# Kernel tuning notes

Hardware: AMD Instinct MI355X
Metric: run time of the kernel (lower is better)

The kernel has to match this reference:

```python
import jax, jax.numpy as jnp
import numpy as np
import math

B, L, DX, DH, DFF, N, M = 16, 1024, 2, 512, 2048, 3, 8
DK = DH // M  # 64
EPS = 1e-5


def batchnorm_pos(z):
    # fresh nn.BatchNorm1d(L, affine=False) in train mode on [B, L, DH]:
    # per-position (dim 1) mean/var over (batch, feature) axes, biased variance
    mu = jnp.mean(z, axis=(0, 2), keepdims=True)
    var = jnp.mean(jnp.square(z - mu), axis=(0, 2), keepdims=True)
    return (z - mu) / jnp.sqrt(var + EPS)


def setup_inputs() -> dict:
    key = jax.random.key(0)
    ks = jax.random.split(key, 13)
    s = lambda k, shape, scale: jax.random.normal(k, shape, dtype=jnp.float32) * scale
    return {
        "x": s(ks[0], (B, L, DX), 1.0),
        "Wh": s(ks[1], (DH, DX), 1.0 / math.sqrt(DX)),
        "bh": s(ks[2], (DH,), 0.02),
        "Wq": s(ks[3], (N, M, DK, DH), 1.0 / math.sqrt(DH)),
        "Wk": s(ks[4], (N, M, DK, DH), 1.0 / math.sqrt(DH)),
        "Wv": s(ks[5], (N, M, DK, DH), 1.0 / math.sqrt(DH)),
        "Wo": s(ks[6], (N, M, DH, DK), 1.0 / math.sqrt(DK)),
        "w_bn": s(ks[7], (N, DH), 1.0),
        "b_bn": s(ks[8], (N, DH), 1.0),
        "Wff0": s(ks[9], (N, DFF, DH), 1.0 / math.sqrt(DH)),
        "bff0": s(ks[10], (N, DFF), 0.02),
        "Wff1": s(ks[11], (N, DH, DFF), 1.0 / math.sqrt(DFF)),
        "bff1": s(ks[12], (N, DH), 0.02),
    }


def reference(x, Wh, bh, Wq, Wk, Wv, Wo, w_bn, b_bn, Wff0, bff0, Wff1, bff1):
    n_layers = Wq.shape[0]
    dk = Wq.shape[2]
    scale = 1.0 / math.sqrt(dk)
    h = jnp.einsum("bld,ed->ble", x, Wh) + bh  # [B, L, DH]
    for n in range(n_layers):
        # batched multi-head attention (replaces per-head python loop)
        q = jnp.einsum("bld,mkd->bmlk", h, Wq[n])  # [B, M, L, DK]
        k = jnp.einsum("bld,mkd->bmlk", h, Wk[n])
        v = jnp.einsum("bld,mvd->bmlv", h, Wv[n])
        scores = jnp.einsum("bmlk,bmjk->bmlj", q, k) * scale  # [B, M, L, L]
        attn = jax.nn.softmax(scores, axis=-1)
        t = jnp.einsum("bmlj,bmjv->bmlv", attn, v)
        h_mha = jnp.einsum("bmlv,mdv->bld", t, Wo[n])  # sum over heads
        h_bn = w_bn[n] * batchnorm_pos(h + h_mha) + b_bn[n]
        ff = jnp.einsum("blf,df->bld", jax.nn.relu(jnp.einsum("bld,fd->blf", h_bn, Wff0[n]) + bff0[n]), Wff1[n]) + bff1[n]
        h = w_bn[n] * batchnorm_pos(h_bn + ff) + b_bn[n]
    return h
```

## Files before the change

### kernel.cpp

```cpp
#include <hip/hip_runtime.h>
#include <hip/hip_bf16.h>
#include <math.h>

#define B_   16
#define L_   1024
#define BL_  16384
#define DH_  512
#define DFF_ 2048
#define NL_  3
#define M_   8
#define DK_  64

typedef __attribute__((ext_vector_type(8))) short bf16x8;
typedef __attribute__((ext_vector_type(4))) float f32x4;
typedef __attribute__((ext_vector_type(4))) unsigned short us4;
typedef __attribute__((ext_vector_type(8))) unsigned short us8;

__device__ __forceinline__ unsigned short f2b(float x) {
    __hip_bfloat16 h = __float2bfloat16(x);
    return *(unsigned short*)&h;
}
__device__ __forceinline__ float b2f(unsigned short u) {
    unsigned int v = ((unsigned int)u) << 16;
    return __builtin_bit_cast(float, v);
}

#define GLDS(g, l) __builtin_amdgcn_global_load_lds( \
        (const __attribute__((address_space(1))) unsigned int*)(const void*)(g), \
        (__attribute__((address_space(3))) unsigned int*)(void*)(l), 16, 0, 0)

#define QKV_T 2359296
#define WO_T  786432
#define FF_T  3145728
__global__ __launch_bounds__(256) void wprep_kernel(
    const float* __restrict__ Wq, const float* __restrict__ Wk,
    const float* __restrict__ Wv, const float* __restrict__ Wo,
    const float* __restrict__ Wff0, const float* __restrict__ Wff1,
    unsigned short* __restrict__ wqkvb3, unsigned short* __restrict__ wob3,
    unsigned short* __restrict__ wff0b3, unsigned short* __restrict__ wff1b3)
{
    int i4 = (blockIdx.x * 256 + threadIdx.x) * 4;
    const float* src;
    unsigned short* dst;
    if (i4 < QKV_T) {
        int n = i4 / 786432, r = i4 % 786432;
        if (r < 262144)      src = Wq + (size_t)n * 262144 + r;
        else if (r < 524288) src = Wk + (size_t)n * 262144 + r - 262144;
        else                 src = Wv + (size_t)n * 262144 + r - 524288;
        dst = wqkvb3 + i4;
    } else if (i4 < QKV_T + WO_T) {
        int i = i4 - QKV_T;
        int n = i / 262144, r = i % 262144;
        int d = r >> 9, mv = r & 511, mm = mv >> 6, vv = mv & 63;
        src = Wo + (size_t)n * 262144 + ((size_t)mm * 512 + d) * 64 + vv;
        dst = wob3 + i;
    } else if (i4 < QKV_T + WO_T + FF_T) {
        int i = i4 - QKV_T - WO_T;
        src = Wff0 + i;
        dst = wff0b3 + i;
    } else {
        int i = i4 - QKV_T - WO_T - FF_T;
        src = Wff1 + i;
        dst = wff1b3 + i;
    }
    float4 v = *(const float4*)src;
    us4 o;
    o.x = f2b(v.x); o.y = f2b(v.y); o.z = f2b(v.z); o.w = f2b(v.w);
    *(us4*)dst = o;
}

__global__ __launch_bounds__(256) void embed_kernel(
    const float* __restrict__ x, const float* __restrict__ Wh,
    const float* __restrict__ bh, unsigned short* __restrict__ hb)
{
    int idx = blockIdx.x * 256 + threadIdx.x;
    int bl = idx >> 7;
    int e0 = (idx & 127) * 4;
    float x0 = x[bl * 2], x1 = x[bl * 2 + 1];
    us4 o;
    #pragma unroll
    for (int r = 0; r < 4; ++r) {
        int e = e0 + r;
        float v = fmaf(x0, Wh[e * 2], fmaf(x1, Wh[e * 2 + 1], bh[e]));
        ((unsigned short*)&o)[r] = f2b(v);
    }
    *(us4*)&hb[(size_t)bl * DH_ + e0] = o;
}

__global__ __launch_bounds__(512, 4) void gemm2w_kernel(
    const unsigned short* __restrict__ A, const unsigned short* __restrict__ Bm,
    const float* __restrict__ bias, unsigned short* __restrict__ Cb,
    unsigned short* __restrict__ vT, int K, int cn, int flags, int gx)
{
    constexpr int SLOT = 32768;
    __shared__ unsigned char lds[2 * SLOT];

    const int tid  = threadIdx.x;
    const int lane = tid & 63, wid = tid >> 6;
    const int wr = wid >> 2, wc = wid & 3;
    const int fr = lane & 15, fq = lane >> 4;

    const int nwg = gridDim.x;
    const int cpx = nwg >> 3;
    const int wg  = blockIdx.x;
    const int swz = (wg & 7) * cpx + (wg >> 3);
    const int by  = swz / gx;
    const int bx  = swz - by * gx;
    const int bm0 = by * 128, bn0 = bx * 128;
    const int cxor = (fr & 7) << 4;

    const int srow  = tid >> 3;
    const int scole = ((tid & 7) ^ (srow & 7)) * 8;
    const unsigned short* Ag = A  + (size_t)(bm0 + srow) * K + scole;
    const unsigned short* Bg = Bm + (size_t)(bn0 + srow) * K + scole;

    f32x4 acc[4][2];
    #pragma unroll
    for (int i = 0; i < 4; ++i)
        #pragma unroll
        for (int j = 0; j < 2; ++j)
            acc[i][j] = (f32x4){0.f, 0.f, 0.f, 0.f};

    auto ldsA = [&](int slot, int sweep) -> void* {
        return (void*)(lds + slot * SLOT + sweep * 8192 + wid * 1024);
    };
    auto ldsB = [&](int slot, int sweep) -> void* {
        return (void*)(lds + slot * SLOT + 16384 + sweep * 8192 + wid * 1024);
    };
    auto srcA = [&](int kt, int sweep) {
        return Ag + (size_t)sweep * 64 * K + kt * 64;
    };
    auto srcB = [&](int kt, int sweep) {
        return Bg + (size_t)sweep * 64 * K + kt * 64;
    };

    const int nt = K >> 6;

    GLDS(srcB(0, 0), ldsB(0, 0)); GLDS(srcB(0, 1), ldsB(0, 1));
    GLDS(srcA(0, 0), ldsA(0, 0)); GLDS(srcA(0, 1), ldsA(0, 1));
    asm volatile("s_waitcnt vmcnt(0)" ::: "memory");
    __builtin_amdgcn_s_barrier();

    for (int kt = 0; kt < nt; ++kt) {
        const int slot = kt & 1;
        const unsigned char* sb = lds + slot * SLOT;
        const int ns = slot ^ 1;
        const bool stg = (kt + 1 < nt);
        const int kn = kt + 1;

        bf16x8 bfr[2][2], af[2][2];
        #pragma unroll
        for (int ni = 0; ni < 2; ++ni)
            #pragma unroll
            for (int kk = 0; kk < 2; ++kk)
                bfr[ni][kk] = *(const bf16x8*)(sb + 16384 +
                    (wc * 32 + ni * 16 + fr) * 128 + ((kk * 64 + fq * 16) ^ cxor));
        #pragma unroll
        for (int mi = 0; mi < 2; ++mi)
            #pragma unroll
            for (int kk = 0; kk < 2; ++kk)
                af[mi][kk] = *(const bf16x8*)(sb +
                    (wr * 64 + mi * 16 + fr) * 128 + ((kk * 64 + fq * 16) ^ cxor));
        if (stg) {
            GLDS(srcB(kn, 0), ldsB(ns, 0)); GLDS(srcB(kn, 1), ldsB(ns, 1));
            GLDS(srcA(kn, 0), ldsA(ns, 0)); GLDS(srcA(kn, 1), ldsA(ns, 1));
        }
        #pragma unroll
        for (int mi = 0; mi < 2; ++mi)
            #pragma unroll
            for (int ni = 0; ni < 2; ++ni) {
                f32x4 c = acc[mi][ni];
                c = __builtin_amdgcn_mfma_f32_16x16x32_bf16(af[mi][0], bfr[ni][0], c, 0, 0, 0);
                c = __builtin_amdgcn_mfma_f32_16x16x32_bf16(af[mi][1], bfr[ni][1], c, 0, 0, 0);
                acc[mi][ni] = c;
            }
        #pragma unroll
        for (int mi = 0; mi < 2; ++mi)
            #pragma unroll
            for (int kk = 0; kk < 2; ++kk)
                af[mi][kk] = *(const bf16x8*)(sb +
                    (wr * 64 + 32 + mi * 16 + fr) * 128 + ((kk * 64 + fq * 16) ^ cxor));
        #pragma unroll
        for (int mi = 0; mi < 2; ++mi)
            #pragma unroll
            for (int ni = 0; ni < 2; ++ni) {
                f32x4 c = acc[2 + mi][ni];
                c = __builtin_amdgcn_mfma_f32_16x16x32_bf16(af[mi][0], bfr[ni][0], c, 0, 0, 0);
                c = __builtin_amdgcn_mfma_f32_16x16x32_bf16(af[mi][1], bfr[ni][1], c, 0, 0, 0);
                acc[2 + mi][ni] = c;
            }
        if (stg) asm volatile("s_waitcnt vmcnt(0)" ::: "memory");
        __builtin_amdgcn_s_barrier();
    }

    float bj[2] = {0.f, 0.f};
    if (flags & 1) {
        #pragma unroll
        for (int ni = 0; ni < 2; ++ni)
            bj[ni] = bias[bn0 + wc * 32 + ni * 16 + fr];
    }
    bool relu = flags & 2;
    bool qkvm = flags & 4;
    #pragma unroll
    for (int am = 0; am < 4; ++am) {
        int row0 = bm0 + wr * 64 + (am >> 1) * 32 + (am & 1) * 16 + fq * 4;
        #pragma unroll
        for (int an = 0; an < 2; ++an) {
            int col = bn0 + wc * 32 + an * 16 + fr;
            float v[4];
            #pragma unroll
            for (int r = 0; r < 4; ++r) {
                v[r] = acc[am][an][r] + bj[an];
                if (relu) v[r] = fmaxf(v[r], 0.f);
            }
            if (qkvm) {
                if (col < 1024) {
                    float sc = (col < 512) ? 0.1803368801111244f : 1.0f;
                    #pragma unroll
                    for (int r = 0; r < 4; ++r)
                        Cb[(size_t)(row0 + r) * cn + col] = f2b(v[r] * sc);
                } else {
                    int mm = (col - 1024) >> 6, dd = (col - 1024) & 63;
                    int bb = row0 >> 10, l0 = row0 & 1023;
                    us4 p;
                    p.x = f2b(v[0]); p.y = f2b(v[1]); p.z = f2b(v[2]); p.w = f2b(v[3]);
                    *(us4*)&vT[((size_t)(bb * 8 + mm) * 64 + dd) * 1024 + l0] = p;
                }
            } else {
                #pragma unroll
                for (int r = 0; r < 4; ++r)
                    Cb[(size_t)(row0 + r) * cn + col] = f2b(v[r]);
            }
        }
    }
}

#define KST 72
__global__ __launch_bounds__(256, 4) void attn_mfma_kernel(
    const unsigned short* __restrict__ qk, const unsigned short* __restrict__ vT,
    unsigned short* __restrict__ t)
{
    __shared__ unsigned short Ks[64 * KST];
    __shared__ unsigned short Vs[64 * KST];
    __shared__ unsigned short Pb[4][32 * KST];

    int tid = threadIdx.x;
    int lane = tid & 63, wid = tid >> 6;
    int fr = lane & 15, fq = lane >> 4;
    int j = blockIdx.x;
    int pair = (j & 7) * 16 + (j >> 6);
    int q0 = ((j >> 3) & 7) * 128;
    int b = pair >> 3, m = pair & 7;
    int bq = b * L_;

    size_t qbase = (size_t)(bq + q0 + wid * 32) * 1024 + m * 64;
    bf16x8 qa[2][2];
    #pragma unroll
    for (int qh = 0; qh < 2; ++qh) {
        qa[qh][0] = *(const bf16x8*)&qk[qbase + (size_t)(qh * 16 + fr) * 1024 + fq * 8];
        qa[qh][1] = *(const bf16x8*)&qk[qbase + (size_t)(qh * 16 + fr) * 1024 + 32 + fq * 8];
    }

    f32x4 oacc[2][4];
    #pragma unroll
    for (int qh = 0; qh < 2; ++qh)
        #pragma unroll
        for (int i = 0; i < 4; ++i) oacc[qh][i] = (f32x4){0.f, 0.f, 0.f, 0.f};
    float lsum[2][4] = {{0.f, 0.f, 0.f, 0.f}, {0.f, 0.f, 0.f, 0.f}};

    int srow = tid >> 3;
    int scol = (tid & 7) * 8;
    const unsigned short* kg = qk + (size_t)bq * 1024 + 512 + m * 64 + scol;
    const unsigned short* vg = vT + ((size_t)pair * 64) * 1024 + scol;
    unsigned short* pw = Pb[wid];

    uint4 k0 = *(const uint4*)&kg[(size_t)(srow) * 1024];
    uint4 k1 = *(const uint4*)&kg[(size_t)(srow + 32) * 1024];
    uint4 v0 = *(const uint4*)&vg[(size_t)(srow) * 1024];
    uint4 v1 = *(const uint4*)&vg[(size_t)(srow + 32) * 1024];

    for (int kt = 0; kt < L_ / 64; ++kt) {
        __syncthreads();
        *(uint4*)&Ks[(srow)      * KST + scol] = k0;
        *(uint4*)&Ks[(srow + 32) * KST + scol] = k1;
        *(uint4*)&Vs[(srow)      * KST + scol] = v0;
        *(uint4*)&Vs[(srow + 32) * KST + scol] = v1;
        __syncthreads();
        if (kt + 1 < L_ / 64) {
            int kb = (kt + 1) * 64;
            k0 = *(const uint4*)&kg[(size_t)(kb + srow) * 1024];
            k1 = *(const uint4*)&kg[(size_t)(kb + srow + 32) * 1024];
            v0 = *(const uint4*)&vg[(size_t)(srow) * 1024 + kb];
            v1 = *(const uint4*)&vg[(size_t)(srow + 32) * 1024 + kb];
        }

        __builtin_amdgcn_s_setprio(1);
        #pragma unroll
        for (int nk = 0; nk < 4; ++nk) {
            bf16x8 kf0 = *(const bf16x8*)&Ks[(nk * 16 + fr) * KST + fq * 8];
            bf16x8 kf1 = *(const bf16x8*)&Ks[(nk * 16 + fr) * KST + 32 + fq * 8];
            #pragma unroll
            for (int qh = 0; qh < 2; ++qh) {
                f32x4 s = __builtin_amdgcn_mfma_f32_16x16x32_bf16(
                    qa[qh][0], kf0, (f32x4){0.f, 0.f, 0.f, 0.f}, 0, 0, 0);
                s = __builtin_amdgcn_mfma_f32_16x16x32_bf16(qa[qh][1], kf1, s, 0, 0, 0);
                #pragma unroll
                for (int r = 0; r < 4; ++r) {
                    float p = exp2f(s[r]);
                    lsum[qh][r] += p;
                    pw[(qh * 16 + fq * 4 + r) * KST + nk * 16 + fr] = f2b(p);
                }
            }
        }
        bf16x8 pa[2][2];
        #pragma unroll
        for (int qh = 0; qh < 2; ++qh) {
            pa[qh][0] = *(const bf16x8*)&pw[(qh * 16 + fr) * KST + fq * 8];
            pa[qh][1] = *(const bf16x8*)&pw[(qh * 16 + fr) * KST + 32 + fq * 8];
        }
        #pragma unroll
        for (int nt = 0; nt < 4; ++nt) {
            bf16x8 vf0 = *(const bf16x8*)&Vs[(nt * 16 + fr) * KST + fq * 8];
            bf16x8 vf1 = *(const bf16x8*)&Vs[(nt * 16 + fr) * KST + 32 + fq * 8];
            #pragma unroll
            for (int qh = 0; qh < 2; ++qh) {
                oacc[qh][nt] = __builtin_amdgcn_mfma_f32_16x16x32_bf16(
                    pa[qh][0], vf0, oacc[qh][nt], 0, 0, 0);
                oacc[qh][nt] = __builtin_amdgcn_mfma_f32_16x16x32_bf16(
                    pa[qh][1], vf1, oacc[qh][nt], 0, 0, 0);
            }
        }
        __builtin_amdgcn_s_setprio(0);
    }

    #pragma unroll
    for (int qh = 0; qh < 2; ++qh)
        #pragma unroll
        for (int r = 0; r < 4; ++r) {
            float s = lsum[qh][r];
            s += __shfl_xor(s, 1); s += __shfl_xor(s, 2);
            s += __shfl_xor(s, 4); s += __shfl_xor(s, 8);
            lsum[qh][r] = 1.f / s;
        }
    #pragma unroll
    for (int qh = 0; qh < 2; ++qh)
        #pragma unroll
        for (int r = 0; r < 4; ++r) {
            size_t orow = (size_t)(bq + q0 + wid * 32 + qh * 16 + fq * 4 + r) * DH_ + m * 64;
            #pragma unroll
            for (int nt = 0; nt < 4; ++nt)
                t[orow + nt * 16 + fr] = f2b(oacc[qh][nt][r] * lsum[qh][r]);
        }
}

__global__ __launch_bounds__(256) void bn_stats_kernel(
    const unsigned short* __restrict__ a, const unsigned short* __restrict__ b,
    float* __restrict__ stats)
{
    int l = blockIdx.x, tid = threadIdx.x;
    float s = 0.f, s2 = 0.f;
    #pragma unroll
    for (int u = tid; u < 1024; u += 256) {
        int bb = u >> 6, dg = (u & 63) * 8;
        size_t off = ((size_t)bb * L_ + l) * DH_ + dg;
        us8 va = *(const us8*)&a[off];
        us8 vb = *(const us8*)&b[off];
        #pragma unroll
        for (int j = 0; j < 8; ++j) {
            float z = b2f(va[j]) + b2f(vb[j]);
            s += z;
            s2 = fmaf(z, z, s2);
        }
    }
    #pragma unroll
    for (int off = 32; off > 0; off >>= 1) {
        s  += __shfl_down(s, off);
        s2 += __shfl_down(s2, off);
    }
    __shared__ float red[8];
    int w = tid >> 6;
    if ((tid & 63) == 0) { red[w] = s; red[4 + w] = s2; }
    __syncthreads();
    if (tid == 0) {
        float S  = red[0] + red[1] + red[2] + red[3];
        float S2 = red[4] + red[5] + red[6] + red[7];
        float mu  = S * (1.f / 8192.f);
        float var = S2 * (1.f / 8192.f) - mu * mu;
        stats[l]      = mu;
        stats[L_ + l] = rsqrtf(var + 1e-5f);
    }
}

__global__ __launch_bounds__(256) void bn_apply_kernel(
    const unsigned short* __restrict__ a, const unsigned short* __restrict__ b,
    const float* __restrict__ stats, const float* __restrict__ w,
    const float* __restrict__ bias, unsigned short* __restrict__ outb,
    float* __restrict__ outf)
{
    int idx = blockIdx.x * 256 + threadIdx.x;
    int bl = idx >> 6;
    int d0 = (idx & 63) * 8;
    int l  = bl & (L_ - 1);
    float mu = stats[l], rs = stats[L_ + l];
    size_t off = (size_t)bl * DH_ + d0;
    us8 va = *(const us8*)&a[off];
    us8 vb = *(const us8*)&b[off];
    float o[8];
    #pragma unroll
    for (int j = 0; j < 8; ++j) {
        float z = b2f(va[j]) + b2f(vb[j]);
        o[j] = fmaf(w[d0 + j], (z - mu) * rs, bias[d0 + j]);
    }
    if (outb) {
        us8 ob;
        #pragma unroll
        for (int j = 0; j < 8; ++j) ob[j] = f2b(o[j]);
        *(us8*)&outb[off] = ob;
    }
    if (outf) {
        float4 o0 = {o[0], o[1], o[2], o[3]};
        float4 o1 = {o[4], o[5], o[6], o[7]};
        *(float4*)&outf[off]     = o0;
        *(float4*)&outf[off + 4] = o1;
    }
}

extern "C" void kernel_launch(void* const* d_in, const int* in_sizes, int n_in,
                              void* d_out, int out_size, void* d_ws, size_t ws_size,
                              hipStream_t stream)
{
    const float* x    = (const float*)d_in[0];
    const float* Wh   = (const float*)d_in[1];
    const float* bh   = (const float*)d_in[2];
    const float* Wq   = (const float*)d_in[3];
    const float* Wk   = (const float*)d_in[4];
    const float* Wv   = (const float*)d_in[5];
    const float* Wo   = (const float*)d_in[6];
    const float* wbn  = (const float*)d_in[7];
    const float* bbn  = (const float*)d_in[8];
    const float* Wff0 = (const float*)d_in[9];
    const float* bff0 = (const float*)d_in[10];
    const float* Wff1 = (const float*)d_in[11];
    const float* bff1 = (const float*)d_in[12];
    float* out = (float*)d_out;

    float* st = (float*)d_ws;
    unsigned short* hb    = (unsigned short*)(st + 2048);
    unsigned short* qkkb  = hb + (size_t)BL_ * DH_;
    unsigned short* vTb   = qkkb + (size_t)BL_ * 1024;
    unsigned short* tb    = vTb + (size_t)BL_ * DH_;
    unsigned short* mhab  = tb + (size_t)BL_ * DH_;
    unsigned short* hbnb  = mhab + (size_t)BL_ * DH_;
    unsigned short* ffob  = hbnb + (size_t)BL_ * DH_;
    unsigned short* wqkvb3 = ffob + (size_t)BL_ * DH_;
    unsigned short* wob3   = wqkvb3 + QKV_T;
    unsigned short* wff0b3 = wob3 + WO_T;
    unsigned short* wff1b3 = wff0b3 + FF_T;
    unsigned short* ffmb  = qkkb;

    wprep_kernel<<<(QKV_T + WO_T + 2 * FF_T) / 1024, 256, 0, stream>>>(
        Wq, Wk, Wv, Wo, Wff0, Wff1, wqkvb3, wob3, wff0b3, wff1b3);
    embed_kernel<<<BL_ * DH_ / 4 / 256, 256, 0, stream>>>(x, Wh, bh, hb);

    const int GQKV = 12 * 128;
    const int GWO  = 4 * 128;
    const int GFF0 = 16 * 128;
    const int GFF1 = 4 * 128;
    int gbn = BL_ * DH_ / 8 / 256;

    for (int n = 0; n < NL_; ++n) {
        const unsigned short* wqkvb = wqkvb3 + (size_t)n * 786432;
        const unsigned short* wob   = wob3   + (size_t)n * 262144;
        const unsigned short* wff0b = wff0b3 + (size_t)n * 1048576;
        const unsigned short* wff1b = wff1b3 + (size_t)n * 1048576;
        const float* wbn_n  = wbn  + (size_t)n * DH_;
        const float* bbn_n  = bbn  + (size_t)n * DH_;
        const float* bff0_n = bff0 + (size_t)n * DFF_;
        const float* bff1_n = bff1 + (size_t)n * DH_;
        bool last = (n == NL_ - 1);

        gemm2w_kernel<<<GQKV, 512, 0, stream>>>(hb, wqkvb, nullptr,
            qkkb, vTb, DH_, 1024, 4, 12);
        attn_mfma_kernel<<<1024, 256, 0, stream>>>(qkkb, vTb, tb);
        gemm2w_kernel<<<GWO, 512, 0, stream>>>(tb, wob, nullptr,
            mhab, nullptr, DH_, DH_, 0, 4);
        bn_stats_kernel<<<L_, 256, 0, stream>>>(hb, mhab, st);
        bn_apply_kernel<<<gbn, 256, 0, stream>>>(hb, mhab, st, wbn_n, bbn_n,
            hbnb, nullptr);
        gemm2w_kernel<<<GFF0, 512, 0, stream>>>(hbnb, wff0b, bff0_n,
            ffmb, nullptr, DH_, DFF_, 1 | 2, 16);
        gemm2w_kernel<<<GFF1, 512, 0, stream>>>(ffmb, wff1b, bff1_n,
            ffob, nullptr, DFF_, DH_, 1, 4);
        bn_stats_kernel<<<L_, 256, 0, stream>>>(hbnb, ffob, st);
        bn_apply_kernel<<<gbn, 256, 0, stream>>>(hbnb, ffob, st, wbn_n, bbn_n,
            last ? nullptr : hb, last ? out : nullptr);
    }
}
```

Measured before the change: 677.7 us.

## Use 4-stage K=32 GEMM pipeline and transposed, XOR-swizzled attention MFMA

The GEMM main loop moves from a 2-slot double buffer with K-tile 64 to a 4-slot ring with K-tile 32. Loads are prefetched two tiles ahead with partial vmcnt waits and MFMA runs at raised priority, so fewer full drains are needed. Attention drops the padded LDS stride in favour of XOR-swizzled K, V and P tiles and swaps the MFMA operand order. This lets each lane hold one query row, so the row sum needs fewer shuffles and the output is written as 4-wide vector stores. The cost is more barriers per K step in the GEMM and extra swizzle address arithmetic.

```diff
diff --git a/kernel.cpp b/kernel.cpp
--- a/kernel.cpp
+++ b/kernel.cpp
@@ -87,13 +87,13 @@
     *(us4*)&hb[(size_t)bl * DH_ + e0] = o;
 }
 
-__global__ __launch_bounds__(512, 4) void gemm2w_kernel(
+__global__ __launch_bounds__(512, 4) void gemm4s_kernel(
     const unsigned short* __restrict__ A, const unsigned short* __restrict__ Bm,
     const float* __restrict__ bias, unsigned short* __restrict__ Cb,
     unsigned short* __restrict__ vT, int K, int cn, int flags, int gx)
 {
-    constexpr int SLOT = 32768;
-    __shared__ unsigned char lds[2 * SLOT];
+    constexpr int SLOT = 16384;
+    __shared__ unsigned char lds[4 * SLOT];
 
     const int tid  = threadIdx.x;
     const int lane = tid & 63, wid = tid >> 6;
@@ -107,10 +107,9 @@
     const int by  = swz / gx;
     const int bx  = swz - by * gx;
     const int bm0 = by * 128, bn0 = bx * 128;
-    const int cxor = (fr & 7) << 4;
-
-    const int srow  = tid >> 3;
-    const int scole = ((tid & 7) ^ (srow & 7)) * 8;
+
+    const int srow  = tid >> 2;
+    const int scole = ((tid & 3) ^ (srow & 3)) * 8;
     const unsigned short* Ag = A  + (size_t)(bm0 + srow) * K + scole;
     const unsigned short* Bg = Bm + (size_t)(bn0 + srow) * K + scole;
 
@@ -121,76 +120,45 @@
         for (int j = 0; j < 2; ++j)
             acc[i][j] = (f32x4){0.f, 0.f, 0.f, 0.f};
 
-    auto ldsA = [&](int slot, int sweep) -> void* {
-        return (void*)(lds + slot * SLOT + sweep * 8192 + wid * 1024);
-    };
-    auto ldsB = [&](int slot, int sweep) -> void* {
-        return (void*)(lds + slot * SLOT + 16384 + sweep * 8192 + wid * 1024);
-    };
-    auto srcA = [&](int kt, int sweep) {
-        return Ag + (size_t)sweep * 64 * K + kt * 64;
-    };
-    auto srcB = [&](int kt, int sweep) {
-        return Bg + (size_t)sweep * 64 * K + kt * 64;
-    };
-
-    const int nt = K >> 6;
-
-    GLDS(srcB(0, 0), ldsB(0, 0)); GLDS(srcB(0, 1), ldsB(0, 1));
-    GLDS(srcA(0, 0), ldsA(0, 0)); GLDS(srcA(0, 1), ldsA(0, 1));
-    asm volatile("s_waitcnt vmcnt(0)" ::: "memory");
+    auto ldsA = [&](int slot) -> void* { return (void*)(lds + slot * SLOT + wid * 1024); };
+    auto ldsB = [&](int slot) -> void* { return (void*)(lds + slot * SLOT + 8192 + wid * 1024); };
+
+    const int nt = K >> 5;
+
+    GLDS(Ag,      ldsA(0)); GLDS(Bg,      ldsB(0));
+    GLDS(Ag + 32, ldsA(1)); GLDS(Bg + 32, ldsB(1));
+    asm volatile("s_waitcnt vmcnt(2)" ::: "memory");
     __builtin_amdgcn_s_barrier();
 
     for (int kt = 0; kt < nt; ++kt) {
-        const int slot = kt & 1;
-        const unsigned char* sb = lds + slot * SLOT;
-        const int ns = slot ^ 1;
-        const bool stg = (kt + 1 < nt);
-        const int kn = kt + 1;
-
-        bf16x8 bfr[2][2], af[2][2];
-        #pragma unroll
-        for (int ni = 0; ni < 2; ++ni)
+        const unsigned char* sb = lds + (kt & 3) * SLOT;
+
+        bf16x8 af[4], bfr[2];
+        #pragma unroll
+        for (int mi = 0; mi < 4; ++mi) {
+            int R = wr * 64 + mi * 16 + fr;
+            af[mi] = *(const bf16x8*)(sb + R * 64 + ((fq ^ (R & 3)) << 4));
+        }
+        #pragma unroll
+        for (int ni = 0; ni < 2; ++ni) {
+            int R = wc * 32 + ni * 16 + fr;
+            bfr[ni] = *(const bf16x8*)(sb + 8192 + R * 64 + ((fq ^ (R & 3)) << 4));
+        }
+        if (kt + 2 < nt) {
+            GLDS(Ag + (kt + 2) * 32, ldsA((kt + 2) & 3));
+            GLDS(Bg + (kt + 2) * 32, ldsB((kt + 2) & 3));
+        }
+        __builtin_amdgcn_s_setprio(1);
+        #pragma unroll
+        for (int mi = 0; mi < 4; ++mi)
             #pragma unroll
-            for (int kk = 0; kk < 2; ++kk)
-                bfr[ni][kk] = *(const bf16x8*)(sb + 16384 +
-                    (wc * 32 + ni * 16 + fr) * 128 + ((kk * 64 + fq * 16) ^ cxor));
-        #pragma unroll
-        for (int mi = 0; mi < 2; ++mi)
-            #pragma unroll
-            for (int kk = 0; kk < 2; ++kk)
-                af[mi][kk] = *(const bf16x8*)(sb +
-                    (wr * 64 + mi * 16 + fr) * 128 + ((kk * 64 + fq * 16) ^ cxor));
-        if (stg) {
-            GLDS(srcB(kn, 0), ldsB(ns, 0)); GLDS(srcB(kn, 1), ldsB(ns, 1));
-            GLDS(srcA(kn, 0), ldsA(ns, 0)); GLDS(srcA(kn, 1), ldsA(ns, 1));
-        }
-        #pragma unroll
-        for (int mi = 0; mi < 2; ++mi)
-            #pragma unroll
-            for (int ni = 0; ni < 2; ++ni) {
-                f32x4 c = acc[mi][ni];
-                c = __builtin_amdgcn_mfma_f32_16x16x32_bf16(af[mi][0], bfr[ni][0], c, 0, 0, 0);
-                c = __builtin_amdgcn_mfma_f32_16x16x32_bf16(af[mi][1], bfr[ni][1], c, 0, 0, 0);
-                acc[mi][ni] = c;
-            }
-        #pragma unroll
-        for (int mi = 0; mi < 2; ++mi)
-            #pragma unroll
-            for (int kk = 0; kk < 2; ++kk)
-                af[mi][kk] = *(const bf16x8*)(sb +
-                    (wr * 64 + 32 + mi * 16 + fr) * 128 + ((kk * 64 + fq * 16) ^ cxor));
-        #pragma unroll
-        for (int mi = 0; mi < 2; ++mi)
-            #pragma unroll
-            for (int ni = 0; ni < 2; ++ni) {
-                f32x4 c = acc[2 + mi][ni];
-                c = __builtin_amdgcn_mfma_f32_16x16x32_bf16(af[mi][0], bfr[ni][0], c, 0, 0, 0);
-                c = __builtin_amdgcn_mfma_f32_16x16x32_bf16(af[mi][1], bfr[ni][1], c, 0, 0, 0);
-                acc[2 + mi][ni] = c;
-            }
-        if (stg) asm volatile("s_waitcnt vmcnt(0)" ::: "memory");
-        __builtin_amdgcn_s_barrier();
+            for (int ni = 0; ni < 2; ++ni)
+                acc[mi][ni] = __builtin_amdgcn_mfma_f32_16x16x32_bf16(
+                    af[mi], bfr[ni], acc[mi][ni], 0, 0, 0);
+        __builtin_amdgcn_s_setprio(0);
+        if (kt + 2 < nt)      asm volatile("s_waitcnt vmcnt(2)" ::: "memory");
+        else if (kt + 1 < nt) asm volatile("s_waitcnt vmcnt(0)" ::: "memory");
+        if (kt + 1 < nt) __builtin_amdgcn_s_barrier();
     }
 
     float bj[2] = {0.f, 0.f};
@@ -202,15 +170,15 @@
     bool relu = flags & 2;
     bool qkvm = flags & 4;
     #pragma unroll
-    for (int am = 0; am < 4; ++am) {
-        int row0 = bm0 + wr * 64 + (am >> 1) * 32 + (am & 1) * 16 + fq * 4;
+    for (int mi = 0; mi < 4; ++mi) {
+        int row0 = bm0 + wr * 64 + mi * 16 + fq * 4;
         #pragma unroll
         for (int an = 0; an < 2; ++an) {
             int col = bn0 + wc * 32 + an * 16 + fr;
             float v[4];
             #pragma unroll
             for (int r = 0; r < 4; ++r) {
-                v[r] = acc[am][an][r] + bj[an];
+                v[r] = acc[mi][an][r] + bj[an];
                 if (relu) v[r] = fmaxf(v[r], 0.f);
             }
             if (qkvm) {
@@ -235,14 +203,13 @@
     }
 }
 
-#define KST 72
 __global__ __launch_bounds__(256, 4) void attn_mfma_kernel(
     const unsigned short* __restrict__ qk, const unsigned short* __restrict__ vT,
     unsigned short* __restrict__ t)
 {
-    __shared__ unsigned short Ks[64 * KST];
-    __shared__ unsigned short Vs[64 * KST];
-    __shared__ unsigned short Pb[4][32 * KST];
+    __shared__ unsigned short Ks[64 * 64];
+    __shared__ unsigned short Vs[64 * 64];
+    __shared__ unsigned short Pb[4][32 * 64];
 
     int tid = threadIdx.x;
     int lane = tid & 63, wid = tid >> 6;
@@ -261,18 +228,20 @@
         qa[qh][1] = *(const bf16x8*)&qk[qbase + (size_t)(qh * 16 + fr) * 1024 + 32 + fq * 8];
     }
 
-    f32x4 oacc[2][4];
+    f32x4 oaccT[2][4];
     #pragma unroll
     for (int qh = 0; qh < 2; ++qh)
         #pragma unroll
-        for (int i = 0; i < 4; ++i) oacc[qh][i] = (f32x4){0.f, 0.f, 0.f, 0.f};
-    float lsum[2][4] = {{0.f, 0.f, 0.f, 0.f}, {0.f, 0.f, 0.f, 0.f}};
+        for (int i = 0; i < 4; ++i) oaccT[qh][i] = (f32x4){0.f, 0.f, 0.f, 0.f};
+    float lsum[2] = {0.f, 0.f};
 
     int srow = tid >> 3;
-    int scol = (tid & 7) * 8;
-    const unsigned short* kg = qk + (size_t)bq * 1024 + 512 + m * 64 + scol;
-    const unsigned short* vg = vT + ((size_t)pair * 64) * 1024 + scol;
+    int c16  = tid & 7;
+    int scole = (c16 ^ (srow & 7)) * 8;
+    const unsigned short* kg = qk + (size_t)bq * 1024 + 512 + m * 64 + scole;
+    const unsigned short* vg = vT + ((size_t)pair * 64) * 1024 + scole;
     unsigned short* pw = Pb[wid];
+    const int u7 = fr & 7;
 
     uint4 k0 = *(const uint4*)&kg[(size_t)(srow) * 1024];
     uint4 k1 = *(const uint4*)&kg[(size_t)(srow + 32) * 1024];
@@ -281,10 +250,10 @@
 
     for (int kt = 0; kt < L_ / 64; ++kt) {
         __syncthreads();
-        *(uint4*)&Ks[(srow)      * KST + scol] = k0;
-        *(uint4*)&Ks[(srow + 32) * KST + scol] = k1;
-        *(uint4*)&Vs[(srow)      * KST + scol] = v0;
-        *(uint4*)&Vs[(srow + 32) * KST + scol] = v1;
+        *(uint4*)&Ks[(srow)      * 64 + c16 * 8] = k0;
+        *(uint4*)&Ks[(srow + 32) * 64 + c16 * 8] = k1;
+        *(uint4*)&Vs[(srow)      * 64 + c16 * 8] = v0;
+        *(uint4*)&Vs[(srow + 32) * 64 + c16 * 8] = v1;
         __syncthreads();
         if (kt + 1 < L_ / 64) {
             int kb = (kt + 1) * 64;
@@ -297,60 +266,71 @@
         __builtin_amdgcn_s_setprio(1);
         #pragma unroll
         for (int nk = 0; nk < 4; ++nk) {
-            bf16x8 kf0 = *(const bf16x8*)&Ks[(nk * 16 + fr) * KST + fq * 8];
-            bf16x8 kf1 = *(const bf16x8*)&Ks[(nk * 16 + fr) * KST + 32 + fq * 8];
+            const unsigned short* krow = &Ks[(nk * 16 + fr) * 64];
+            bf16x8 kf0 = *(const bf16x8*)&krow[((fq     ) ^ u7) * 8];
+            bf16x8 kf1 = *(const bf16x8*)&krow[((4 + fq) ^ u7) * 8];
             #pragma unroll
             for (int qh = 0; qh < 2; ++qh) {
                 f32x4 s = __builtin_amdgcn_mfma_f32_16x16x32_bf16(
-                    qa[qh][0], kf0, (f32x4){0.f, 0.f, 0.f, 0.f}, 0, 0, 0);
-                s = __builtin_amdgcn_mfma_f32_16x16x32_bf16(qa[qh][1], kf1, s, 0, 0, 0);
+                    kf0, qa[qh][0], (f32x4){0.f, 0.f, 0.f, 0.f}, 0, 0, 0);
+                s = __builtin_amdgcn_mfma_f32_16x16x32_bf16(kf1, qa[qh][1], s, 0, 0, 0);
+                us4 pk;
                 #pragma unroll
                 for (int r = 0; r < 4; ++r) {
                     float p = exp2f(s[r]);
-                    lsum[qh][r] += p;
-                    pw[(qh * 16 + fq * 4 + r) * KST + nk * 16 + fr] = f2b(p);
+                    lsum[qh] += p;
+                    ((unsigned short*)&pk)[r] = f2b(p);
                 }
+                int prow = qh * 16 + fr;
+                int pc16 = nk * 2 + (fq >> 1);
+                int addr = prow * 128 + ((pc16 ^ (prow & 7)) << 4) + (fq & 1) * 8;
+                *(us4*)((unsigned char*)pw + addr) = pk;
             }
         }
         bf16x8 pa[2][2];
         #pragma unroll
         for (int qh = 0; qh < 2; ++qh) {
-            pa[qh][0] = *(const bf16x8*)&pw[(qh * 16 + fr) * KST + fq * 8];
-            pa[qh][1] = *(const bf16x8*)&pw[(qh * 16 + fr) * KST + 32 + fq * 8];
+            int prow = qh * 16 + fr;
+            const unsigned char* pr = (const unsigned char*)pw + prow * 128;
+            pa[qh][0] = *(const bf16x8*)(pr + (((fq    ) ^ (prow & 7)) << 4));
+            pa[qh][1] = *(const bf16x8*)(pr + (((4 + fq) ^ (prow & 7)) << 4));
         }
         #pragma unroll
         for (int nt = 0; nt < 4; ++nt) {
-            bf16x8 vf0 = *(const bf16x8*)&Vs[(nt * 16 + fr) * KST + fq * 8];
-            bf16x8 vf1 = *(const bf16x8*)&Vs[(nt * 16 + fr) * KST + 32 + fq * 8];
+            const unsigned short* vrow = &Vs[(nt * 16 + fr) * 64];
+            bf16x8 vf0 = *(const bf16x8*)&vrow[((fq     ) ^ u7) * 8];
+            bf16x8 vf1 = *(const bf16x8*)&vrow[((4 + fq) ^ u7) * 8];
             #pragma unroll
             for (int qh = 0; qh < 2; ++qh) {
-                oacc[qh][nt] = __builtin_amdgcn_mfma_f32_16x16x32_bf16(
-                    pa[qh][0], vf0, oacc[qh][nt], 0, 0, 0);
-                oacc[qh][nt] = __builtin_amdgcn_mfma_f32_16x16x32_bf16(
-                    pa[qh][1], vf1, oacc[qh][nt], 0, 0, 0);
+                oaccT[qh][nt] = __builtin_amdgcn_mfma_f32_16x16x32_bf16(
+                    vf0, pa[qh][0], oaccT[qh][nt], 0, 0, 0);
+                oaccT[qh][nt] = __builtin_amdgcn_mfma_f32_16x16x32_bf16(
+                    vf1, pa[qh][1], oaccT[qh][nt], 0, 0, 0);
             }
         }
         __builtin_amdgcn_s_setprio(0);
     }
 
-    #pragma unroll
-    for (int qh = 0; qh < 2; ++qh)
-        #pragma unroll
-        for (int r = 0; r < 4; ++r) {
-            float s = lsum[qh][r];
-            s += __shfl_xor(s, 1); s += __shfl_xor(s, 2);
-            s += __shfl_xor(s, 4); s += __shfl_xor(s, 8);
-            lsum[qh][r] = 1.f / s;
-        }
-    #pragma unroll
-    for (int qh = 0; qh < 2; ++qh)
-        #pragma unroll
-        for (int r = 0; r < 4; ++r) {
-            size_t orow = (size_t)(bq + q0 + wid * 32 + qh * 16 + fq * 4 + r) * DH_ + m * 64;
+    float inv[2];
+    #pragma unroll
+    for (int qh = 0; qh < 2; ++qh) {
+        float s = lsum[qh];
+        s += __shfl_xor(s, 16);
+        s += __shfl_xor(s, 32);
+        inv[qh] = 1.f / s;
+    }
+    #pragma unroll
+    for (int qh = 0; qh < 2; ++qh) {
+        size_t orow = (size_t)(bq + q0 + wid * 32 + qh * 16 + fr) * DH_ + m * 64;
+        #pragma unroll
+        for (int nt = 0; nt < 4; ++nt) {
+            us4 ob;
             #pragma unroll
-            for (int nt = 0; nt < 4; ++nt)
-                t[orow + nt * 16 + fr] = f2b(oacc[qh][nt][r] * lsum[qh][r]);
-        }
+            for (int r = 0; r < 4; ++r)
+                ((unsigned short*)&ob)[r] = f2b(oaccT[qh][nt][r] * inv[qh]);
+            *(us4*)&t[orow + nt * 16 + fq * 4] = ob;
+        }
+    }
 }
 
 __global__ __launch_bounds__(256) void bn_stats_kernel(
@@ -479,17 +459,17 @@
         const float* bff1_n = bff1 + (size_t)n * DH_;
         bool last = (n == NL_ - 1);
 
-        gemm2w_kernel<<<GQKV, 512, 0, stream>>>(hb, wqkvb, nullptr,
+        gemm4s_kernel<<<GQKV, 512, 0, stream>>>(hb, wqkvb, nullptr,
             qkkb, vTb, DH_, 1024, 4, 12);
         attn_mfma_kernel<<<1024, 256, 0, stream>>>(qkkb, vTb, tb);
-        gemm2w_kernel<<<GWO, 512, 0, stream>>>(tb, wob, nullptr,
+        gemm4s_kernel<<<GWO, 512, 0, stream>>>(tb, wob, nullptr,
             mhab, nullptr, DH_, DH_, 0, 4);
         bn_stats_kernel<<<L_, 256, 0, stream>>>(hb, mhab, st);
         bn_apply_kernel<<<gbn, 256, 0, stream>>>(hb, mhab, st, wbn_n, bbn_n,
             hbnb, nullptr);
-        gemm2w_kernel<<<GFF0, 512, 0, stream>>>(hbnb, wff0b, bff0_n,
+        gemm4s_kernel<<<GFF0, 512, 0, stream>>>(hbnb, wff0b, bff0_n,
             ffmb, nullptr, DH_, DFF_, 1 | 2, 16);
-        gemm2w_kernel<<<GFF1, 512, 0, stream>>>(ffmb, wff1b, bff1_n,
+        gemm4s_kernel<<<GFF1, 512, 0, stream>>>(ffmb, wff1b, bff1_n,
             ffob, nullptr, DFF_, DH_, 1, 4);
         bn_stats_kernel<<<L_, 256, 0, stream>>>(hbnb, ffob, st);
         bn_apply_kernel<<<gbn, 256, 0, stream>>>(hbnb, ffob, st, wbn_n, bbn_n,
```

Result: slower. 700.1 us (+3.3%).

## Swizzle attention LDS tiles and transpose MFMA operands for vectorized P/output stores

Applied to the files above, without the earlier changes.

The attention kernel drops padded LDS rows in favour of XOR-swizzled 64-element rows for K, V and P. It swaps the MFMA operand order so each lane holds four consecutive key or feature columns. That lets P be written to LDS and the output written to global memory as 8-byte vectors instead of scalar shorts, and it reduces the row-sum reduction to two shuffles. Separately, the GEMM kernel now issues its next-tile global-to-LDS loads before the LDS fragment reads rather than after. This adds address arithmetic and depends on the swizzle being consistent between the writers and readers.

```diff
diff --git a/kernel.cpp b/kernel.cpp
--- a/kernel.cpp
+++ b/kernel.cpp
@@ -148,6 +148,10 @@
         const bool stg = (kt + 1 < nt);
         const int kn = kt + 1;
 
+        if (stg) {
+            GLDS(srcB(kn, 0), ldsB(ns, 0)); GLDS(srcB(kn, 1), ldsB(ns, 1));
+            GLDS(srcA(kn, 0), ldsA(ns, 0)); GLDS(srcA(kn, 1), ldsA(ns, 1));
+        }
         bf16x8 bfr[2][2], af[2][2];
         #pragma unroll
         for (int ni = 0; ni < 2; ++ni)
@@ -161,10 +165,6 @@
             for (int kk = 0; kk < 2; ++kk)
                 af[mi][kk] = *(const bf16x8*)(sb +
                     (wr * 64 + mi * 16 + fr) * 128 + ((kk * 64 + fq * 16) ^ cxor));
-        if (stg) {
-            GLDS(srcB(kn, 0), ldsB(ns, 0)); GLDS(srcB(kn, 1), ldsB(ns, 1));
-            GLDS(srcA(kn, 0), ldsA(ns, 0)); GLDS(srcA(kn, 1), ldsA(ns, 1));
-        }
         #pragma unroll
         for (int mi = 0; mi < 2; ++mi)
             #pragma unroll
@@ -235,14 +235,13 @@
     }
 }
 
-#define KST 72
 __global__ __launch_bounds__(256, 4) void attn_mfma_kernel(
     const unsigned short* __restrict__ qk, const unsigned short* __restrict__ vT,
     unsigned short* __restrict__ t)
 {
-    __shared__ unsigned short Ks[64 * KST];
-    __shared__ unsigned short Vs[64 * KST];
-    __shared__ unsigned short Pb[4][32 * KST];
+    __shared__ unsigned short Ks[64 * 64];
+    __shared__ unsigned short Vs[64 * 64];
+    __shared__ unsigned short Pb[4][32 * 64];
 
     int tid = threadIdx.x;
     int lane = tid & 63, wid = tid >> 6;
@@ -261,18 +260,20 @@
         qa[qh][1] = *(const bf16x8*)&qk[qbase + (size_t)(qh * 16 + fr) * 1024 + 32 + fq * 8];
     }
 
-    f32x4 oacc[2][4];
+    f32x4 oaccT[2][4];
     #pragma unroll
     for (int qh = 0; qh < 2; ++qh)
         #pragma unroll
-        for (int i = 0; i < 4; ++i) oacc[qh][i] = (f32x4){0.f, 0.f, 0.f, 0.f};
-    float lsum[2][4] = {{0.f, 0.f, 0.f, 0.f}, {0.f, 0.f, 0.f, 0.f}};
+        for (int i = 0; i < 4; ++i) oaccT[qh][i] = (f32x4){0.f, 0.f, 0.f, 0.f};
+    float lsum[2] = {0.f, 0.f};
 
     int srow = tid >> 3;
-    int scol = (tid & 7) * 8;
-    const unsigned short* kg = qk + (size_t)bq * 1024 + 512 + m * 64 + scol;
-    const unsigned short* vg = vT + ((size_t)pair * 64) * 1024 + scol;
+    int c16  = tid & 7;
+    int scole = (c16 ^ (srow & 7)) * 8;
+    const unsigned short* kg = qk + (size_t)bq * 1024 + 512 + m * 64 + scole;
+    const unsigned short* vg = vT + ((size_t)pair * 64) * 1024 + scole;
     unsigned short* pw = Pb[wid];
+    const int u7 = fr & 7;
 
     uint4 k0 = *(const uint4*)&kg[(size_t)(srow) * 1024];
     uint4 k1 = *(const uint4*)&kg[(size_t)(srow + 32) * 1024];
@@ -281,10 +282,10 @@
 
     for (int kt = 0; kt < L_ / 64; ++kt) {
         __syncthreads();
-        *(uint4*)&Ks[(srow)      * KST + scol] = k0;
-        *(uint4*)&Ks[(srow + 32) * KST + scol] = k1;
-        *(uint4*)&Vs[(srow)      * KST + scol] = v0;
-        *(uint4*)&Vs[(srow + 32) * KST + scol] = v1;
+        *(uint4*)&Ks[(srow)      * 64 + c16 * 8] = k0;
+        *(uint4*)&Ks[(srow + 32) * 64 + c16 * 8] = k1;
+        *(uint4*)&Vs[(srow)      * 64 + c16 * 8] = v0;
+        *(uint4*)&Vs[(srow + 32) * 64 + c16 * 8] = v1;
         __syncthreads();
         if (kt + 1 < L_ / 64) {
             int kb = (kt + 1) * 64;
@@ -297,60 +298,71 @@
         __builtin_amdgcn_s_setprio(1);
         #pragma unroll
         for (int nk = 0; nk < 4; ++nk) {
-            bf16x8 kf0 = *(const bf16x8*)&Ks[(nk * 16 + fr) * KST + fq * 8];
-            bf16x8 kf1 = *(const bf16x8*)&Ks[(nk * 16 + fr) * KST + 32 + fq * 8];
+            const unsigned short* krow = &Ks[(nk * 16 + fr) * 64];
+            bf16x8 kf0 = *(const bf16x8*)&krow[((fq     ) ^ u7) * 8];
+            bf16x8 kf1 = *(const bf16x8*)&krow[((4 + fq) ^ u7) * 8];
             #pragma unroll
             for (int qh = 0; qh < 2; ++qh) {
                 f32x4 s = __builtin_amdgcn_mfma_f32_16x16x32_bf16(
-                    qa[qh][0], kf0, (f32x4){0.f, 0.f, 0.f, 0.f}, 0, 0, 0);
-                s = __builtin_amdgcn_mfma_f32_16x16x32_bf16(qa[qh][1], kf1, s, 0, 0, 0);
+                    kf0, qa[qh][0], (f32x4){0.f, 0.f, 0.f, 0.f}, 0, 0, 0);
+                s = __builtin_amdgcn_mfma_f32_16x16x32_bf16(kf1, qa[qh][1], s, 0, 0, 0);
+                us4 pk;
                 #pragma unroll
                 for (int r = 0; r < 4; ++r) {
                     float p = exp2f(s[r]);
-                    lsum[qh][r] += p;
-                    pw[(qh * 16 + fq * 4 + r) * KST + nk * 16 + fr] = f2b(p);
+                    lsum[qh] += p;
+                    ((unsigned short*)&pk)[r] = f2b(p);
                 }
+                int prow = qh * 16 + fr;
+                int pc16 = nk * 2 + (fq >> 1);
+                int addr = prow * 128 + ((pc16 ^ (prow & 7)) << 4) + (fq & 1) * 8;
+                *(us4*)((unsigned char*)pw + addr) = pk;
             }
         }
         bf16x8 pa[2][2];
         #pragma unroll
         for (int qh = 0; qh < 2; ++qh) {
-            pa[qh][0] = *(const bf16x8*)&pw[(qh * 16 + fr) * KST + fq * 8];
-            pa[qh][1] = *(const bf16x8*)&pw[(qh * 16 + fr) * KST + 32 + fq * 8];
+            int prow = qh * 16 + fr;
+            const unsigned char* pr = (const unsigned char*)pw + prow * 128;
+            pa[qh][0] = *(const bf16x8*)(pr + (((fq    ) ^ (prow & 7)) << 4));
+            pa[qh][1] = *(const bf16x8*)(pr + (((4 + fq) ^ (prow & 7)) << 4));
         }
         #pragma unroll
         for (int nt = 0; nt < 4; ++nt) {
-            bf16x8 vf0 = *(const bf16x8*)&Vs[(nt * 16 + fr) * KST + fq * 8];
-            bf16x8 vf1 = *(const bf16x8*)&Vs[(nt * 16 + fr) * KST + 32 + fq * 8];
+            const unsigned short* vrow = &Vs[(nt * 16 + fr) * 64];
+            bf16x8 vf0 = *(const bf16x8*)&vrow[((fq     ) ^ u7) * 8];
+            bf16x8 vf1 = *(const bf16x8*)&vrow[((4 + fq) ^ u7) * 8];
             #pragma unroll
             for (int qh = 0; qh < 2; ++qh) {
-                oacc[qh][nt] = __builtin_amdgcn_mfma_f32_16x16x32_bf16(
-                    pa[qh][0], vf0, oacc[qh][nt], 0, 0, 0);
-                oacc[qh][nt] = __builtin_amdgcn_mfma_f32_16x16x32_bf16(
-                    pa[qh][1], vf1, oacc[qh][nt], 0, 0, 0);
+                oaccT[qh][nt] = __builtin_amdgcn_mfma_f32_16x16x32_bf16(
+                    vf0, pa[qh][0], oaccT[qh][nt], 0, 0, 0);
+                oaccT[qh][nt] = __builtin_amdgcn_mfma_f32_16x16x32_bf16(
+                    vf1, pa[qh][1], oaccT[qh][nt], 0, 0, 0);
             }
         }
         __builtin_amdgcn_s_setprio(0);
     }
 
-    #pragma unroll
-    for (int qh = 0; qh < 2; ++qh)
-        #pragma unroll
-        for (int r = 0; r < 4; ++r) {
-            float s = lsum[qh][r];
-            s += __shfl_xor(s, 1); s += __shfl_xor(s, 2);
-            s += __shfl_xor(s, 4); s += __shfl_xor(s, 8);
-            lsum[qh][r] = 1.f / s;
-        }
-    #pragma unroll
-    for (int qh = 0; qh < 2; ++qh)
-        #pragma unroll
-        for (int r = 0; r < 4; ++r) {
-            size_t orow = (size_t)(bq + q0 + wid * 32 + qh * 16 + fq * 4 + r) * DH_ + m * 64;
-            #pragma unroll
-            for (int nt = 0; nt < 4; ++nt)
-                t[orow + nt * 16 + fr] = f2b(oacc[qh][nt][r] * lsum[qh][r]);
-        }
+    float inv[2];
+    #pragma unroll
+    for (int qh = 0; qh < 2; ++qh) {
+        float s = lsum[qh];
+        s += __shfl_xor(s, 16);
+        s += __shfl_xor(s, 32);
+        inv[qh] = 1.f / s;
+    }
+    #pragma unroll
+    for (int qh = 0; qh < 2; ++qh) {
+        size_t orow = (size_t)(bq + q0 + wid * 32 + qh * 16 + fr) * DH_ + m * 64;
+        #pragma unroll
+        for (int nt = 0; nt < 4; ++nt) {
+            us4 ob;
+            #pragma unroll
+            for (int r = 0; r < 4; ++r)
+                ((unsigned short*)&ob)[r] = f2b(oaccT[qh][nt][r] * inv[qh]);
+            *(us4*)&t[orow + nt * 16 + fq * 4] = ob;
+        }
+    }
 }
 
 __global__ __launch_bounds__(256) void bn_stats_kernel(
```

Measured after the change: 656.6 us. 1.03x faster.
